# Kernel optimization log

Hardware: AMD Instinct MI355X
Metric: run time of the kernel (lower is better)

The kernel has to match this reference:

```python
import jax, jax.numpy as jnp
import numpy as np

ETYPES = [0, 2, 1]          # indexes into doubled RotatE0 r_vec (2*R rows)
OUT_DIM = 64
NUM_HEADS = 8
ALPHA = 0.01                # LeakyReLU slope
R = 2                       # raw relation count (r_vec rows before doubling)
N = 100000                  # num nodes
E = 250000                  # num edges (metapath instances)
L = len(ETYPES) + 1         # metapath length


def setup_inputs() -> dict:
    key = jax.random.key(0)
    k = jax.random.split(key, 6)
    features = jax.random.normal(k[0], (N, OUT_DIM), jnp.float32)
    r_vec = jax.random.normal(k[1], (R, OUT_DIM // 2, 2), jnp.float32)
    attn1_w = jax.random.normal(k[2], (NUM_HEADS, OUT_DIM), jnp.float32) * 0.1
    attn2 = jax.random.normal(k[3], (1, NUM_HEADS, OUT_DIM), jnp.float32) * 0.1
    edge_metapath_indices = jax.random.randint(k[4], (E, L), 0, N)
    edge_dst = jax.random.randint(k[5], (E,), 0, N)
    return {"features": features, "r_vec": r_vec, "attn1_w": attn1_w,
            "attn2": attn2, "edge_metapath_indices": edge_metapath_indices,
            "edge_dst": edge_dst}


def _forward(features, r_vec, attn1_w, attn2, edge_metapath_indices, edge_dst):
    D2 = OUT_DIM // 2
    # --- RotatE0 relation vectors: normalize each complex pair to unit length ---
    rv = r_vec / jnp.linalg.norm(r_vec, axis=2, keepdims=True)      # [R, D2, 2]
    rv_conj = rv * jnp.array([1.0, -1.0], rv.dtype)                 # conjugate
    rv2 = jnp.stack((rv, rv_conj), axis=1).reshape(2 * R, D2, 2)    # [2R, D2, 2]
    # --- cumulative rotation per metapath position (reverse product) ---
    fr = [None] * L
    fr[L - 1] = jnp.stack([jnp.ones(D2, rv.dtype), jnp.zeros(D2, rv.dtype)], -1)
    for i in range(L - 2, -1, -1):
        if ETYPES[i] is not None:
            r = rv2[ETYPES[i]]                                       # [D2, 2]
            re = fr[i + 1][:, 0] * r[:, 0] - fr[i + 1][:, 1] * r[:, 1]
            im = fr[i + 1][:, 0] * r[:, 1] + fr[i + 1][:, 1] * r[:, 0]
            fr[i] = jnp.stack([re, im], axis=-1)
        else:
            fr[i] = fr[i + 1]
    frv = jnp.stack(fr, axis=0)                                      # [L, D2, 2]
    # --- gather node features along each metapath instance ---
    edata = features[edge_metapath_indices]                          # [E, L, D]
    ed = edata.reshape(edata.shape[0], L, D2, 2)
    # position L-1 has identity rotation (1,0), so rotate all positions at once
    re = ed[..., 0] * frv[None, :, :, 0] - ed[..., 1] * frv[None, :, :, 1]
    im = ed[..., 0] * frv[None, :, :, 1] + ed[..., 1] * frv[None, :, :, 0]
    ed = jnp.stack([re, im], axis=-1).reshape(edata.shape[0], L, OUT_DIM)
    hidden = ed.mean(axis=1)                                         # [E, D]
    eft = jnp.tile(hidden, (1, NUM_HEADS)).reshape(-1, NUM_HEADS, OUT_DIM)
    # --- attention scores (attn_switch=True) ---
    center = features[edge_metapath_indices[:, -1]]                  # [E, D]
    a1 = center @ attn1_w.T                                          # [E, H]
    a2 = (eft * attn2).sum(axis=-1)                                  # [E, H]
    a = a1 + a2
    a = jnp.where(a > 0, a, ALPHA * a)[:, :, None]                   # leaky relu, [E,H,1]
    # --- edge softmax over destination-node segments ---
    amax = jax.lax.stop_gradient(jax.ops.segment_max(a, edge_dst, num_segments=N))
    aexp = jnp.exp(a - amax[edge_dst])
    asum = jax.ops.segment_sum(aexp, edge_dst, num_segments=N)
    attn = aexp / asum[edge_dst]                                     # [E, H, 1]
    # --- message passing: weighted scatter-sum to destination nodes ---
    h = jax.ops.segment_sum(eft * attn, edge_dst, num_segments=N)    # [N, H, D]
    return h


def reference(features, r_vec, attn1_w, attn2, edge_metapath_indices, edge_dst):
    return _forward(features, r_vec, attn1_w, attn2, edge_metapath_indices, edge_dst)
```

## Files before the change

### kernel.cpp

```cpp
#include <hip/hip_runtime.h>

#define NUM_HEADS 8

__device__ __forceinline__ float2 cmul(float2 a, float2 b) {
    return make_float2(a.x*b.x - a.y*b.y, a.x*b.y + a.y*b.x);
}

__global__ __launch_bounds__(256) void k_pre(
    const float2* __restrict__ feat,
    const float2* __restrict__ rvec,
    const float2* __restrict__ w1_g,
    const float2* __restrict__ w2_g,
    float*        __restrict__ P, int N)
{
    int tid = threadIdx.x;
    int lane = tid & 31;
    int l = lane >> 3, h = lane & 7;

    float2 Wr[32];
    for (int d = 0; d < 32; ++d) {
        float2 a = rvec[d], b = rvec[32 + d];
        float na = rsqrtf(a.x*a.x + a.y*a.y); a.x *= na; a.y *= na;
        float nb = rsqrtf(b.x*b.x + b.y*b.y); b.x *= nb; b.y *= nb;
        float2 fr2 = make_float2(a.x, -a.y);
        float2 fr1 = cmul(fr2, b);
        float2 fr0 = cmul(fr1, a);
        float2 fr = (l == 0) ? fr0 : (l == 1) ? fr1 : (l == 2) ? fr2 : make_float2(1.f, 0.f);
        float2 frc = make_float2(fr.x, -fr.y);
        float2 w2 = w2_g[h*32 + d];
        float2 wl = cmul(w2, frc);
        wl.x *= 0.25f; wl.y *= 0.25f;
        if (l == 3) { float2 w1 = w1_g[h*32 + d]; wl.x += w1.x; wl.y += w1.y; }
        Wr[d] = wl;
    }

    int g = tid >> 5;
    for (int n = blockIdx.x * 8 + g; n < N; n += gridDim.x * 8) {
        const float4* f4 = (const float4*)(feat + (size_t)n * 32);
        float acc = 0.f;
        #pragma unroll
        for (int q = 0; q < 16; ++q) {
            float4 v = f4[q];
            acc += v.x * Wr[2*q].x + v.y * Wr[2*q].y
                 + v.z * Wr[2*q+1].x + v.w * Wr[2*q+1].y;
        }
        P[(size_t)n * 32 + lane] = acc;
    }
}

__global__ void k_count(const int* __restrict__ edge_dst, int* __restrict__ counts, int E) {
    int e = blockIdx.x * 256 + threadIdx.x;
    if (e < E) atomicAdd(&counts[edge_dst[e]], 1);
}

__global__ __launch_bounds__(256) void k_scan_a(
    const int* __restrict__ counts, int* __restrict__ offsets,
    int* __restrict__ blocksums, int N)
{
    __shared__ int s[256];
    int t = threadIdx.x;
    int base = blockIdx.x * 1024 + t * 4;
    int v0 = (base     < N) ? counts[base]     : 0;
    int v1 = (base + 1 < N) ? counts[base + 1] : 0;
    int v2 = (base + 2 < N) ? counts[base + 2] : 0;
    int v3 = (base + 3 < N) ? counts[base + 3] : 0;
    s[t] = v0 + v1 + v2 + v3;
    __syncthreads();
    #pragma unroll
    for (int off = 1; off < 256; off <<= 1) {
        int x = (t >= off) ? s[t - off] : 0;
        __syncthreads();
        s[t] += x;
        __syncthreads();
    }
    if (t == 255) blocksums[blockIdx.x] = s[255];
    int run = (t == 0) ? 0 : s[t - 1];
    if (base     < N) offsets[base]     = run; run += v0;
    if (base + 1 < N) offsets[base + 1] = run; run += v1;
    if (base + 2 < N) offsets[base + 2] = run; run += v2;
    if (base + 3 < N) offsets[base + 3] = run;
}

__global__ __launch_bounds__(1024) void k_scan_b(
    int* __restrict__ blocksums, int* __restrict__ total, int B)
{
    __shared__ int s[1024];
    int t = threadIdx.x;
    s[t] = (t < B) ? blocksums[t] : 0;
    __syncthreads();
    #pragma unroll
    for (int off = 1; off < 1024; off <<= 1) {
        int x = (t >= off) ? s[t - off] : 0;
        __syncthreads();
        s[t] += x;
        __syncthreads();
    }
    if (t < B) blocksums[t] = (t == 0) ? 0 : s[t - 1];
    if (t == 1023) *total = s[1023];
}

__global__ __launch_bounds__(256) void k_scan_c(
    int* __restrict__ offsets, int* __restrict__ cursor,
    const int* __restrict__ blocksums, const int* __restrict__ total, int N)
{
    int i = blockIdx.x * 256 + threadIdx.x;
    if (i < N) {
        int v = offsets[i] + blocksums[i >> 10];
        offsets[i] = v;
        cursor[i] = v;
    }
    if (i == 0) offsets[N] = *total;
}

__global__ void k_fill(const int* __restrict__ edge_dst, int* __restrict__ cursor,
                       const int4* __restrict__ emi, int4* __restrict__ emi_perm, int E) {
    int e = blockIdx.x * 256 + threadIdx.x;
    if (e >= E) return;
    int pos = atomicAdd(&cursor[edge_dst[e]], 1);
    emi_perm[pos] = emi[e];
}

__global__ __launch_bounds__(256) void k_out(
    const float2* __restrict__ feat,
    const float2* __restrict__ rvec,
    const float*  __restrict__ P,
    const int*    __restrict__ offsets,
    const int4*   __restrict__ emi_perm,
    float2*       __restrict__ out,
    int N)
{
    __shared__ float2 s_frv[96];
    int tid = threadIdx.x;
    if (tid < 32) {
        float2 a = rvec[tid], b = rvec[32 + tid];
        float na = rsqrtf(a.x*a.x + a.y*a.y); a.x *= na; a.y *= na;
        float nb = rsqrtf(b.x*b.x + b.y*b.y); b.x *= nb; b.y *= nb;
        float2 fr2 = make_float2(a.x, -a.y);
        float2 fr1 = cmul(fr2, b);
        float2 fr0 = cmul(fr1, a);
        s_frv[tid] = fr0; s_frv[32 + tid] = fr1; s_frv[64 + tid] = fr2;
    }
    __syncthreads();

    int n = blockIdx.x * 8 + (tid >> 5);
    if (n >= N) return;
    int lane = tid & 31;
    int beg = offsets[n], end = offsets[n + 1];

    if (beg == end) {
        float2 z = make_float2(0.f, 0.f);
        #pragma unroll
        for (int hh = 0; hh < NUM_HEADS; ++hh)
            out[((size_t)n * 8 + hh) * 32 + lane] = z;
        return;
    }

    float2 fr0 = s_frv[lane], fr1 = s_frv[32 + lane], fr2 = s_frv[64 + lane];

    float dsum[NUM_HEADS];
    float2 acc[NUM_HEADS];
    #pragma unroll
    for (int hh = 0; hh < NUM_HEADS; ++hh) { dsum[hh] = 0.f; acc[hh] = make_float2(0.f, 0.f); }

    for (int j = beg; j < end; ++j) {
        int4 idx = emi_perm[j];

        const float4* q0 = (const float4*)(P + (size_t)idx.x * 32);
        const float4* q1 = (const float4*)(P + (size_t)idx.y * 32 + 8);
        const float4* q2 = (const float4*)(P + (size_t)idx.z * 32 + 16);
        const float4* q3 = (const float4*)(P + (size_t)idx.w * 32 + 24);
        float4 u0 = q0[0], v0 = q0[1];
        float4 u1 = q1[0], v1 = q1[1];
        float4 u2 = q2[0], v2 = q2[1];
        float4 u3 = q3[0], v3 = q3[1];
        float aw[NUM_HEADS];
        aw[0] = u0.x + u1.x + u2.x + u3.x;
        aw[1] = u0.y + u1.y + u2.y + u3.y;
        aw[2] = u0.z + u1.z + u2.z + u3.z;
        aw[3] = u0.w + u1.w + u2.w + u3.w;
        aw[4] = v0.x + v1.x + v2.x + v3.x;
        aw[5] = v0.y + v1.y + v2.y + v3.y;
        aw[6] = v0.z + v1.z + v2.z + v3.z;
        aw[7] = v0.w + v1.w + v2.w + v3.w;

        float2 f0 = feat[(size_t)idx.x * 32 + lane];
        float2 f1 = feat[(size_t)idx.y * 32 + lane];
        float2 f2 = feat[(size_t)idx.z * 32 + lane];
        float2 c3 = feat[(size_t)idx.w * 32 + lane];
        float2 hv;
        hv.x = c3.x + f0.x*fr0.x - f0.y*fr0.y
                    + f1.x*fr1.x - f1.y*fr1.y
                    + f2.x*fr2.x - f2.y*fr2.y;
        hv.y = c3.y + f0.x*fr0.y + f0.y*fr0.x
                    + f1.x*fr1.y + f1.y*fr1.x
                    + f2.x*fr2.y + f2.y*fr2.x;
        hv.x *= 0.25f; hv.y *= 0.25f;

        #pragma unroll
        for (int hh = 0; hh < NUM_HEADS; ++hh) {
            float av = aw[hh];
            av = av > 0.f ? av : 0.01f * av;
            float wgt = __expf(av);
            dsum[hh] += wgt;
            acc[hh].x += wgt * hv.x;
            acc[hh].y += wgt * hv.y;
        }
    }

    #pragma unroll
    for (int hh = 0; hh < NUM_HEADS; ++hh) {
        float r = 1.f / dsum[hh];
        out[((size_t)n * 8 + hh) * 32 + lane] = make_float2(acc[hh].x * r, acc[hh].y * r);
    }
}

extern "C" void kernel_launch(void* const* d_in, const int* in_sizes, int n_in,
                              void* d_out, int out_size, void* d_ws, size_t ws_size,
                              hipStream_t stream) {
    const float2* feat = (const float2*)d_in[0];
    const float2* rvec = (const float2*)d_in[1];
    const float2* w1   = (const float2*)d_in[2];
    const float2* w2   = (const float2*)d_in[3];
    const int4*   emi  = (const int4*)d_in[4];
    const int* edge_dst = (const int*)d_in[5];

    int N = in_sizes[0] / 64;
    int E = in_sizes[4] / 4;
    int nTiles = (N + 1023) / 1024;

    char* w = (char*)d_ws;
    float* P        = (float*)w;
    int4*  emi_perm = (int4*)(P + (size_t)N * 32);
    int*   counts   = (int*)(emi_perm + E);
    int*   offsets  = counts + N;
    int*   cursor   = offsets + N + 1;
    int*   blocksums= cursor + N;
    int*   total    = blocksums + 1024;

    hipMemsetAsync(counts, 0, (size_t)N * 4, stream);

    k_count<<<(E + 255) / 256, 256, 0, stream>>>(edge_dst, counts, E);
    k_pre<<<(N + 63) / 64, 256, 0, stream>>>(feat, rvec, w1, w2, P, N);
    k_scan_a<<<nTiles, 256, 0, stream>>>(counts, offsets, blocksums, N);
    k_scan_b<<<1, 1024, 0, stream>>>(blocksums, total, nTiles);
    k_scan_c<<<(N + 255) / 256, 256, 0, stream>>>(offsets, cursor, blocksums, total, N);
    k_fill<<<(E + 255) / 256, 256, 0, stream>>>(edge_dst, cursor, emi, emi_perm, E);
    k_out<<<(N + 7) / 8, 256, 0, stream>>>(feat, rvec, P, offsets, emi_perm,
                                           (float2*)d_out, N);
}
```

Measured before the change: 394.0 us.

## Move per-edge hidden and attention computation into edge kernel writing CSR-ordered buffer

Replaces the index-permutation fill kernel with an edge-parallel kernel that gathers metapath features, computes the rotated hidden vector and exponentiated attention weights, and writes them into a per-edge row at its destination-sorted position. The output kernel then streams these contiguous rows per destination node instead of doing random gathers inside a serial per-node loop. The precompute kernel also stages its 64-node feature tile in shared memory before the dot products. The idea is to turn latency-bound dependent gathers in the output loop into parallel edge work and coalesced reads. The cost is an extra intermediate buffer of about 288 bytes per edge that must be written and read back.

```diff
diff --git a/kernel.cpp b/kernel.cpp
--- a/kernel.cpp
+++ b/kernel.cpp
@@ -7,12 +7,13 @@
 }
 
 __global__ __launch_bounds__(256) void k_pre(
-    const float2* __restrict__ feat,
+    const float4* __restrict__ feat4,
     const float2* __restrict__ rvec,
     const float2* __restrict__ w1_g,
     const float2* __restrict__ w2_g,
     float*        __restrict__ P, int N)
 {
+    __shared__ float4 sf[1024];
     int tid = threadIdx.x;
     int lane = tid & 31;
     int l = lane >> 3, h = lane & 7;
@@ -34,13 +35,22 @@
         Wr[d] = wl;
     }
 
-    int g = tid >> 5;
-    for (int n = blockIdx.x * 8 + g; n < N; n += gridDim.x * 8) {
-        const float4* f4 = (const float4*)(feat + (size_t)n * 32);
+    int n0 = blockIdx.x * 64;
+    int lim = (N - n0) * 16;
+    for (int i = tid; i < 1024; i += 256)
+        sf[i] = (i < lim) ? feat4[(size_t)n0 * 16 + i] : make_float4(0.f, 0.f, 0.f, 0.f);
+    __syncthreads();
+
+    int grp = tid >> 5;
+    #pragma unroll
+    for (int k = 0; k < 8; ++k) {
+        int n = n0 + grp * 8 + k;
+        if (n >= N) break;
+        const float4* fp = &sf[(grp * 8 + k) * 16];
         float acc = 0.f;
         #pragma unroll
         for (int q = 0; q < 16; ++q) {
-            float4 v = f4[q];
+            float4 v = fp[q];
             acc += v.x * Wr[2*q].x + v.y * Wr[2*q].y
                  + v.z * Wr[2*q+1].x + v.w * Wr[2*q+1].y;
         }
@@ -112,22 +122,15 @@
     if (i == 0) offsets[N] = *total;
 }
 
-__global__ void k_fill(const int* __restrict__ edge_dst, int* __restrict__ cursor,
-                       const int4* __restrict__ emi, int4* __restrict__ emi_perm, int E) {
-    int e = blockIdx.x * 256 + threadIdx.x;
-    if (e >= E) return;
-    int pos = atomicAdd(&cursor[edge_dst[e]], 1);
-    emi_perm[pos] = emi[e];
-}
-
-__global__ __launch_bounds__(256) void k_out(
+__global__ __launch_bounds__(256) void k_edge(
     const float2* __restrict__ feat,
     const float2* __restrict__ rvec,
     const float*  __restrict__ P,
-    const int*    __restrict__ offsets,
-    const int4*   __restrict__ emi_perm,
-    float2*       __restrict__ out,
-    int N)
+    const int4*   __restrict__ emi,
+    const int*    __restrict__ edge_dst,
+    int*          __restrict__ cursor,
+    float2*       __restrict__ hbuf,
+    int E)
 {
     __shared__ float2 s_frv[96];
     int tid = threadIdx.x;
@@ -142,6 +145,50 @@
     }
     __syncthreads();
 
+    int e = blockIdx.x * 8 + (tid >> 5);
+    if (e >= E) return;
+    int lane = tid & 31;
+
+    int4 idx = emi[e];
+    int pos = 0;
+    if (lane == 0) pos = atomicAdd(&cursor[edge_dst[e]], 1);
+    pos = __shfl(pos, 0, 32);
+
+    float2 f0 = feat[(size_t)idx.x * 32 + lane];
+    float2 f1 = feat[(size_t)idx.y * 32 + lane];
+    float2 f2 = feat[(size_t)idx.z * 32 + lane];
+    float2 c3 = feat[(size_t)idx.w * 32 + lane];
+    float2 fr0 = s_frv[lane], fr1 = s_frv[32 + lane], fr2 = s_frv[64 + lane];
+
+    float2 hv;
+    hv.x = c3.x + f0.x*fr0.x - f0.y*fr0.y
+                + f1.x*fr1.x - f1.y*fr1.y
+                + f2.x*fr2.x - f2.y*fr2.y;
+    hv.y = c3.y + f0.x*fr0.y + f0.y*fr0.x
+                + f1.x*fr1.y + f1.y*fr1.x
+                + f2.x*fr2.y + f2.y*fr2.x;
+    hv.x *= 0.25f; hv.y *= 0.25f;
+
+    float2* row = hbuf + (size_t)pos * 36;
+    row[lane] = hv;
+
+    if (lane < NUM_HEADS) {
+        float a = P[(size_t)idx.x * 32 + lane]
+                + P[(size_t)idx.y * 32 +  8 + lane]
+                + P[(size_t)idx.z * 32 + 16 + lane]
+                + P[(size_t)idx.w * 32 + 24 + lane];
+        a = a > 0.f ? a : 0.01f * a;
+        ((float*)(row + 32))[lane] = __expf(a);
+    }
+}
+
+__global__ __launch_bounds__(256) void k_out(
+    const float2* __restrict__ hbuf,
+    const int*    __restrict__ offsets,
+    float2*       __restrict__ out,
+    int N)
+{
+    int tid = threadIdx.x;
     int n = blockIdx.x * 8 + (tid >> 5);
     if (n >= N) return;
     int lane = tid & 31;
@@ -155,56 +202,24 @@
         return;
     }
 
-    float2 fr0 = s_frv[lane], fr1 = s_frv[32 + lane], fr2 = s_frv[64 + lane];
-
     float dsum[NUM_HEADS];
     float2 acc[NUM_HEADS];
     #pragma unroll
     for (int hh = 0; hh < NUM_HEADS; ++hh) { dsum[hh] = 0.f; acc[hh] = make_float2(0.f, 0.f); }
 
     for (int j = beg; j < end; ++j) {
-        int4 idx = emi_perm[j];
-
-        const float4* q0 = (const float4*)(P + (size_t)idx.x * 32);
-        const float4* q1 = (const float4*)(P + (size_t)idx.y * 32 + 8);
-        const float4* q2 = (const float4*)(P + (size_t)idx.z * 32 + 16);
-        const float4* q3 = (const float4*)(P + (size_t)idx.w * 32 + 24);
-        float4 u0 = q0[0], v0 = q0[1];
-        float4 u1 = q1[0], v1 = q1[1];
-        float4 u2 = q2[0], v2 = q2[1];
-        float4 u3 = q3[0], v3 = q3[1];
-        float aw[NUM_HEADS];
-        aw[0] = u0.x + u1.x + u2.x + u3.x;
-        aw[1] = u0.y + u1.y + u2.y + u3.y;
-        aw[2] = u0.z + u1.z + u2.z + u3.z;
-        aw[3] = u0.w + u1.w + u2.w + u3.w;
-        aw[4] = v0.x + v1.x + v2.x + v3.x;
-        aw[5] = v0.y + v1.y + v2.y + v3.y;
-        aw[6] = v0.z + v1.z + v2.z + v3.z;
-        aw[7] = v0.w + v1.w + v2.w + v3.w;
-
-        float2 f0 = feat[(size_t)idx.x * 32 + lane];
-        float2 f1 = feat[(size_t)idx.y * 32 + lane];
-        float2 f2 = feat[(size_t)idx.z * 32 + lane];
-        float2 c3 = feat[(size_t)idx.w * 32 + lane];
-        float2 hv;
-        hv.x = c3.x + f0.x*fr0.x - f0.y*fr0.y
-                    + f1.x*fr1.x - f1.y*fr1.y
-                    + f2.x*fr2.x - f2.y*fr2.y;
-        hv.y = c3.y + f0.x*fr0.y + f0.y*fr0.x
-                    + f1.x*fr1.y + f1.y*fr1.x
-                    + f2.x*fr2.y + f2.y*fr2.x;
-        hv.x *= 0.25f; hv.y *= 0.25f;
-
-        #pragma unroll
-        for (int hh = 0; hh < NUM_HEADS; ++hh) {
-            float av = aw[hh];
-            av = av > 0.f ? av : 0.01f * av;
-            float wgt = __expf(av);
-            dsum[hh] += wgt;
-            acc[hh].x += wgt * hv.x;
-            acc[hh].y += wgt * hv.y;
-        }
+        const float2* row = hbuf + (size_t)j * 36;
+        float2 hv = row[lane];
+        float4 wa = ((const float4*)(row + 32))[0];
+        float4 wb = ((const float4*)(row + 32))[1];
+        dsum[0] += wa.x; acc[0].x += wa.x * hv.x; acc[0].y += wa.x * hv.y;
+        dsum[1] += wa.y; acc[1].x += wa.y * hv.x; acc[1].y += wa.y * hv.y;
+        dsum[2] += wa.z; acc[2].x += wa.z * hv.x; acc[2].y += wa.z * hv.y;
+        dsum[3] += wa.w; acc[3].x += wa.w * hv.x; acc[3].y += wa.w * hv.y;
+        dsum[4] += wb.x; acc[4].x += wb.x * hv.x; acc[4].y += wb.x * hv.y;
+        dsum[5] += wb.y; acc[5].x += wb.y * hv.x; acc[5].y += wb.y * hv.y;
+        dsum[6] += wb.z; acc[6].x += wb.z * hv.x; acc[6].y += wb.z * hv.y;
+        dsum[7] += wb.w; acc[7].x += wb.w * hv.x; acc[7].y += wb.w * hv.y;
     }
 
     #pragma unroll
@@ -229,22 +244,22 @@
     int nTiles = (N + 1023) / 1024;
 
     char* w = (char*)d_ws;
-    float* P        = (float*)w;
-    int4*  emi_perm = (int4*)(P + (size_t)N * 32);
-    int*   counts   = (int*)(emi_perm + E);
-    int*   offsets  = counts + N;
-    int*   cursor   = offsets + N + 1;
-    int*   blocksums= cursor + N;
-    int*   total    = blocksums + 1024;
+    float*  P        = (float*)w;
+    float2* hbuf     = (float2*)(P + (size_t)N * 32);
+    int*    counts   = (int*)(hbuf + (size_t)E * 36);
+    int*    offsets  = counts + N;
+    int*    cursor   = offsets + N + 1;
+    int*    blocksums= cursor + N;
+    int*    total    = blocksums + 1024;
 
     hipMemsetAsync(counts, 0, (size_t)N * 4, stream);
 
     k_count<<<(E + 255) / 256, 256, 0, stream>>>(edge_dst, counts, E);
-    k_pre<<<(N + 63) / 64, 256, 0, stream>>>(feat, rvec, w1, w2, P, N);
+    k_pre<<<(N + 63) / 64, 256, 0, stream>>>((const float4*)feat, rvec, w1, w2, P, N);
     k_scan_a<<<nTiles, 256, 0, stream>>>(counts, offsets, blocksums, N);
     k_scan_b<<<1, 1024, 0, stream>>>(blocksums, total, nTiles);
     k_scan_c<<<(N + 255) / 256, 256, 0, stream>>>(offsets, cursor, blocksums, total, N);
-    k_fill<<<(E + 255) / 256, 256, 0, stream>>>(edge_dst, cursor, emi, emi_perm, E);
-    k_out<<<(N + 7) / 8, 256, 0, stream>>>(feat, rvec, P, offsets, emi_perm,
-                                           (float2*)d_out, N);
-}
+    k_edge<<<(E + 7) / 8, 256, 0, stream>>>(feat, rvec, P, emi, edge_dst, cursor,
+                                            hbuf, E);
+    k_out<<<(N + 7) / 8, 256, 0, stream>>>(hbuf, offsets, (float2*)d_out, N);
+}
```

Result: slower. 406.1 us (+3.1%).
